# Kernel optimization log

Measured on AMD Instinct MI355X. Metric: run time of the kernel, lower is better.

Reference implementation:

```python
import jax, jax.numpy as jnp
import numpy as np

B, N, E = 2, 50000, 800000
IN_CH, SP_CH, OUT_CH, EDGE_CH = 64, 16, 32, 1


def _xavier(k, shape):
    scale = (2.0 / (shape[0] + shape[1])) ** 0.5
    return jax.random.normal(k, shape, dtype=jnp.float32) * scale


def setup_inputs() -> dict:
    key = jax.random.key(0)
    ks = jax.random.split(key, 20)
    return {
        "X": jax.random.normal(ks[0], (B, N, IN_CH), dtype=jnp.float32),
        "edge_index0": jax.random.randint(ks[1], (2, E), 0, N),
        "edge_index1": jax.random.randint(ks[2], (2, E), 0, N),
        "edge_weight0": jax.random.uniform(ks[3], (E, EDGE_CH), dtype=jnp.float32),
        "edge_weight1": jax.random.uniform(ks[4], (E, EDGE_CH), dtype=jnp.float32),
        "res_n_id0": jnp.arange(N),
        "res_n_id1": jnp.arange(N),
        # conv1 params (in=IN_CH, out=SP_CH)
        "value1": _xavier(ks[5], (IN_CH, SP_CH)),
        "key1": _xavier(ks[6], (SP_CH, SP_CH)),
        "query1": _xavier(ks[7], (SP_CH, SP_CH)),
        "we1": _xavier(ks[8], (EDGE_CH, SP_CH)),
        "att_w1": _xavier(ks[9], (3 * SP_CH, 1)),
        "att_b1": jnp.zeros((1,), jnp.float32),
        "cat_w1": _xavier(ks[10], (2 * SP_CH, SP_CH)),
        "cat_b1": jnp.zeros((SP_CH,), jnp.float32),
        # conv2 params (in=SP_CH, out=OUT_CH)
        "value2": _xavier(ks[11], (SP_CH, OUT_CH)),
        "key2": _xavier(ks[12], (OUT_CH, OUT_CH)),
        "query2": _xavier(ks[13], (OUT_CH, OUT_CH)),
        "we2": _xavier(ks[14], (EDGE_CH, OUT_CH)),
        "att_w2": _xavier(ks[15], (3 * OUT_CH, 1)),
        "att_b2": jnp.zeros((1,), jnp.float32),
        "cat_w2": _xavier(ks[16], (2 * OUT_CH, OUT_CH)),
        "cat_b2": jnp.zeros((OUT_CH,), jnp.float32),
    }


def _egnn_conv(Xs, Xd, ei, ef, value, key_w, query_w, we, att_w, att_b, cat_w, cat_b):
    # Xs: [B,Ns,Cin] source nodes, Xd: [B,Nd,Cin] dest nodes, ei: [2,E], ef: [E,edge_ch]
    xs = Xs @ value                       # [B,Ns,C]
    xd = Xd @ value                       # [B,Nd,C]
    e = ef @ we                           # [E,C]
    xj = xs[:, ei[0]]                     # [B,E,C] source gather
    xi = xd[:, ei[1]]                     # [B,E,C] dest gather
    q = xj @ query_w                      # note: original code names are swapped; kept faithful
    k = xi @ key_w
    att_in = jnp.concatenate([k, q, jnp.broadcast_to(e, q.shape)], axis=-1)  # [B,E,3C]
    att = jax.nn.sigmoid(att_in @ att_w + att_b)      # [B,E,1]
    msg = att * xj * jax.nn.sigmoid(e)                # [B,E,C]
    aggr = jnp.zeros(xd.shape, xd.dtype).at[:, ei[1]].add(msg)  # scatter-add over dest
    upd = jnp.concatenate([xd, aggr], axis=-1) @ cat_w + cat_b  # [B,Nd,C]
    return xd + jax.nn.relu(upd)


def reference(X, edge_index0, edge_index1, edge_weight0, edge_weight1,
              res_n_id0, res_n_id1,
              value1, key1, query1, we1, att_w1, att_b1, cat_w1, cat_b1,
              value2, key2, query2, we2, att_w2, att_b2, cat_w2, cat_b2):
    X1 = _egnn_conv(X, X[:, res_n_id0], edge_index0, edge_weight0,
                    value1, key1, query1, we1, att_w1, att_b1, cat_w1, cat_b1)
    X1 = jax.nn.leaky_relu(X1)  # negative_slope 0.01, matches torch default
    X2 = _egnn_conv(X1, X1[:, res_n_id1], edge_index1, edge_weight1,
                    value2, key2, query2, we2, att_w2, att_b2, cat_w2, cat_b2)
    return X2
```

## Files before the change

kernel.cpp:

```cpp
#include <hip/hip_runtime.h>
#include <hip/hip_fp16.h>

#define BB   2
#define NN   50000
#define EE   800000
#define INCH 64
#define C1   16
#define C2   32
#define NB   (BB*NN)

#define W1S   6
#define W2S   5
#define NBK1  ((NN + 63) >> 6)
#define NBK2  ((NN + 31) >> 5)
#define NBKT  (NBK1 + NBK2)
#define EB    4096
#define TPB   1024
#define NEBLK ((2*EE + EB - 1) / EB)

#define OFF_XS1   0
#define OFF_XS2   (OFF_XS1 + NB*C1/2)
#define OFF_DOTK1 (OFF_XS2 + NB*C2/2)
#define OFF_DOTQ1 (OFF_DOTK1 + NB)
#define OFF_DOTK2 (OFF_DOTQ1 + NB)
#define OFF_DOTQ2 (OFF_DOTK2 + NB)
#define OFF_AG1   (OFF_DOTQ2 + NB)
#define OFF_AG2   (OFF_AG1 + NN*32)
#define OFF_BTOT  (OFF_AG2 + NN*64)
#define OFF_BBASE (OFF_BTOT + NBKT)
#define OFF_START (OFF_BBASE + NBKT)
#define OFF_DEG   (OFF_START + 2*NN)
#define OFF_SC    (OFF_DEG + 2*NN)
#define OFF_RECS2 (OFF_SC + 2)
#define OFF_REGION (OFF_RECS2 + 2*EE*2)
#define OFF_RECS   OFF_REGION
#define OFF_BCNT   (OFF_REGION + 2*EE*2)
#define OFF_PREC   OFF_REGION

__device__ __forceinline__ float sigmoidf(float x) {
    return __builtin_amdgcn_rcpf(1.0f + __expf(-x));
}

__device__ __forceinline__ float h2f_u(unsigned u) {
    return __half2float(__ushort_as_half((unsigned short)u));
}

__global__ __launch_bounds__(TPB) void k_value1cnt(
        const float* __restrict__ X, const float* __restrict__ value1,
        const float* __restrict__ key1, const float* __restrict__ query1,
        const float* __restrict__ aw1,
        const int* __restrict__ ei0, const int* __restrict__ ei1,
        const float* __restrict__ we1, const float* __restrict__ we2,
        const float* __restrict__ aw2,
        __half* __restrict__ xs1h, float* __restrict__ dotk1,
        float* __restrict__ dotq1, unsigned* __restrict__ blockCnt,
        float* __restrict__ sc) {
    __shared__ float W[INCH*C1];
    __shared__ float KV[C1], QV[C1];
    __shared__ unsigned h[NBKT];
    int tid = threadIdx.x;
    if (tid < 256) {
        for (int i = tid; i < INCH*C1; i += 256) W[i] = value1[i];
        if (tid < C1) {
            float kv = 0.f, qv = 0.f;
#pragma unroll
            for (int j = 0; j < C1; ++j) {
                kv += key1[tid*C1+j]   * aw1[j];
                qv += query1[tid*C1+j] * aw1[C1+j];
            }
            KV[tid] = kv; QV[tid] = qv;
        }
    } else {
        for (int i = tid - 256; i < NBKT; i += 768) h[i] = 0u;
        if (blockIdx.x == 0 && tid == 256) {
            float e = 0.f;
            for (int j = 0; j < C1; ++j) e += we1[j] * aw1[2*C1+j];
            sc[0] = e;
        }
        if (blockIdx.x == 0 && tid == 257) {
            float e = 0.f;
            for (int j = 0; j < C2; ++j) e += we2[j] * aw2[2*C2+j];
            sc[1] = e;
        }
    }
    __syncthreads();
    if (tid < 256) {
        int bn = blockIdx.x * 256 + tid;
        if (bn < NB) {
            int b = (bn >= NN) ? 1 : 0;
            int node = bn - b*NN;
            const float4* Xr = (const float4*)(X + (size_t)bn * INCH);
            float acc[C1];
#pragma unroll
            for (int j = 0; j < C1; ++j) acc[j] = 0.f;
#pragma unroll
            for (int v = 0; v < 16; ++v) {
                float4 p = Xr[v];
                float x4[4] = {p.x, p.y, p.z, p.w};
#pragma unroll
                for (int hh = 0; hh < 4; ++hh) {
                    int i = v*4 + hh;
                    float xv = x4[hh];
#pragma unroll
                    for (int j = 0; j < C1; ++j) acc[j] += xv * W[i*C1+j];
                }
            }
            float dk = 0.f, dq = 0.f;
#pragma unroll
            for (int j = 0; j < C1; ++j) { dk += acc[j]*KV[j]; dq += acc[j]*QV[j]; }
            __half* o = xs1h + ((size_t)node * C1) * 2 + b;
#pragma unroll
            for (int j = 0; j < C1; ++j) o[2*j] = __float2half_rn(acc[j]);
            dotk1[node*2 + b] = dk; dotq1[node*2 + b] = dq;
        }
    } else {
        int base = blockIdx.x * EB;
        for (int j = tid - 256; j < EB; j += 768) {
            int t = base + j;
            if (t < 2*EE) {
                int bkt;
                if (t < EE) { int dst = ei0[EE + t];      bkt = dst >> W1S; }
                else        { int dst = ei1[EE + t - EE]; bkt = NBK1 + (dst >> W2S); }
                atomicAdd(&h[bkt], 1u);
            }
        }
    }
    __syncthreads();
    unsigned* o = blockCnt + (size_t)blockIdx.x * NBKT;
    for (int i = tid; i < NBKT; i += TPB) o[i] = h[i];
}

__global__ __launch_bounds__(512) void k_scanBkt(
        unsigned* __restrict__ blockCnt, unsigned* __restrict__ bktTot) {
    __shared__ unsigned s[512];
    int tid = threadIdx.x;
    int bkt = blockIdx.x;
    unsigned v = (tid < NEBLK) ? blockCnt[(size_t)tid * NBKT + bkt] : 0u;
    s[tid] = v;
    __syncthreads();
    for (int o = 1; o < 512; o <<= 1) {
        unsigned t = (tid >= o) ? s[tid - o] : 0u;
        __syncthreads();
        s[tid] += t;
        __syncthreads();
    }
    if (tid < NEBLK) blockCnt[(size_t)tid * NBKT + bkt] = s[tid] - v;
    if (tid == 511) bktTot[bkt] = s[511];
}

__global__ __launch_bounds__(1024) void k_scanTot(
        const unsigned* __restrict__ bktTot, unsigned* __restrict__ bucketBase) {
    __shared__ unsigned s[1024];
    int tid = threadIdx.x;
    int base = tid * 3;
    unsigned a0 = (base + 0 < NBKT) ? bktTot[base + 0] : 0u;
    unsigned a1 = (base + 1 < NBKT) ? bktTot[base + 1] : 0u;
    unsigned a2 = (base + 2 < NBKT) ? bktTot[base + 2] : 0u;
    unsigned l = a0 + a1 + a2;
    s[tid] = l;
    __syncthreads();
    for (int o = 1; o < 1024; o <<= 1) {
        unsigned t = (tid >= o) ? s[tid - o] : 0u;
        __syncthreads();
        s[tid] += t;
        __syncthreads();
    }
    unsigned ex = s[tid] - l;
    if (base + 0 < NBKT) bucketBase[base + 0] = ex;
    if (base + 1 < NBKT) bucketBase[base + 1] = ex + a0;
    if (base + 2 < NBKT) bucketBase[base + 2] = ex + a0 + a1;
}

__global__ __launch_bounds__(TPB) void k_permute(
        const int* __restrict__ ei0, const int* __restrict__ ei1,
        const float* __restrict__ ew0, const float* __restrict__ ew1,
        const unsigned* __restrict__ blockOff, const unsigned* __restrict__ bucketBase,
        uint2* __restrict__ recs) {
    __shared__ unsigned off[NBKT];
    __shared__ unsigned cur[NBKT];
    int tid = threadIdx.x;
    const unsigned* bo = blockOff + (size_t)blockIdx.x * NBKT;
    for (int i = tid; i < NBKT; i += TPB) { off[i] = bo[i] + bucketBase[i]; cur[i] = 0u; }
    __syncthreads();
    int base = blockIdx.x * EB;
#pragma unroll
    for (int j = 0; j < EB/TPB; ++j) {
        int t = base + j*TPB + tid;
        if (t >= 2*EE) break;
        int bkt, dl, src; float ef;
        if (t < EE) {
            int dst = ei0[EE + t];
            bkt = dst >> W1S; dl = dst & 63;
            src = ei0[t]; ef = ew0[t];
        } else {
            int e = t - EE;
            int dst = ei1[EE + e];
            bkt = NBK1 + (dst >> W2S); dl = dst & 31;
            src = ei1[e]; ef = ew1[e];
        }
        unsigned pos = off[bkt] + atomicAdd(&cur[bkt], 1u);
        recs[pos] = make_uint2((unsigned)src | ((unsigned)dl << 16), __float_as_uint(ef));
    }
}

__global__ __launch_bounds__(256) void k_sortbp(
        const uint2* __restrict__ recs, const unsigned* __restrict__ bktTot,
        const unsigned* __restrict__ bucketBase,
        const float* __restrict__ dotk1, const float* __restrict__ dotq1,
        const float* __restrict__ ab1, const float* __restrict__ sc,
        uint2* __restrict__ recs2, unsigned* __restrict__ startA,
        unsigned* __restrict__ degA) {
    __shared__ unsigned h[64], sOff[64], cur[64];
    int tid = threadIdx.x;
    int bkt = blockIdx.x;
    int lay1 = (bkt < NBK1) ? 1 : 0;
    int ndl  = lay1 ? 64 : 32;
    int nodeBase = lay1 ? (bkt << W1S) : ((bkt - NBK1) << W2S);
    int layOff   = lay1 ? 0 : NN;
    if (tid < 64) h[tid] = 0u;
    __syncthreads();
    unsigned cnt = bktTot[bkt], base = bucketBase[bkt];
    for (unsigned i = tid; i < cnt; i += 256)
        atomicAdd(&h[recs[base + i].x >> 16], 1u);
    __syncthreads();
    if (tid == 0) {
        unsigned run = 0;
        for (int d = 0; d < ndl; ++d) { sOff[d] = run; run += h[d]; }
    }
    __syncthreads();
    if (tid < ndl) {
        cur[tid] = sOff[tid];
        int node = nodeBase + tid;
        if (node < NN) {
            startA[layOff + node] = base + sOff[tid];
            degA[layOff + node]   = h[tid];
        }
    }
    __syncthreads();
    float ec = sc[0], ab0 = ab1[0];
    for (unsigned i = tid; i < cnt; i += 256) {
        uint2 r = recs[base + i];
        unsigned dl  = r.x >> 16;
        unsigned src = r.x & 0xffffu;
        unsigned pos = atomicAdd(&cur[dl], 1u);
        unsigned dst = (unsigned)nodeBase + dl;
        if (lay1) {
            float ef = __uint_as_float(r.y);
            float eb = ef * ec + ab0;
            float2 dk = *(const float2*)(dotk1 + dst*2);
            float2 dq = *(const float2*)(dotq1 + src*2);
            float p0 = sigmoidf(dk.x + dq.x + eb);
            float p1 = sigmoidf(dk.y + dq.y + eb);
            unsigned pu = __builtin_bit_cast(unsigned, __floats2half2_rn(p0, p1));
            unsigned eu = (unsigned)__half_as_ushort(__float2half_rn(ef));
            recs2[base + pos] = make_uint2(src | (pu << 16),
                                           (pu >> 16) | (eu << 16));
        } else {
            recs2[base + pos] = make_uint2(src | (dst << 16), r.y);
        }
    }
}

__global__ __launch_bounds__(256) void k_prep(
        const uint2* __restrict__ recs2seg, const float* __restrict__ dotk,
        const float* __restrict__ dotq, const float* __restrict__ ab,
        const float* __restrict__ sc, int scIdx, uint2* __restrict__ prec) {
    int e = blockIdx.x * 256 + threadIdx.x;
    uint2 r = recs2seg[e];
    int src = r.x & 0xffff, dst = r.x >> 16;
    float ef = __uint_as_float(r.y);
    float eb = ef * sc[scIdx] + ab[0];
    float2 dk = *(const float2*)(dotk + dst*2);
    float2 dq = *(const float2*)(dotq + src*2);
    float p0 = sigmoidf(dk.x + dq.x + eb);
    float p1 = sigmoidf(dk.y + dq.y + eb);
    unsigned pu = __builtin_bit_cast(unsigned, __floats2half2_rn(p0, p1));
    unsigned eu = (unsigned)__half_as_ushort(__float2half_rn(ef));
    prec[e] = make_uint2((unsigned)src | (pu << 16),
                         (pu >> 16) | (eu << 16));
}

__global__ __launch_bounds__(256) void k_aggr1u(
        const uint2* __restrict__ prec, const float* __restrict__ we,
        const uint2* __restrict__ xsh,
        const unsigned* __restrict__ startA, const unsigned* __restrict__ degA,
        const float* __restrict__ cat_w, const float* __restrict__ cat_b,
        const float* __restrict__ value2,
        const float* __restrict__ key2, const float* __restrict__ query2,
        const float* __restrict__ aw2, const __half* __restrict__ xs1h,
        __half* __restrict__ xs2h, float* __restrict__ dotk2,
        float* __restrict__ dotq2) {
    __shared__ float CW[2*C1*C1];
    __shared__ float CB[C1];
    __shared__ float V2[C1*C2];
    __shared__ float KV[C2], QV[C2];
    __shared__ float agS[16*36];
    __shared__ float xdS[16*2*17];
    __shared__ float x1S[16*2*17];
    int tid = threadIdx.x;
    for (int i = tid; i < 2*C1*C1; i += 256) CW[i] = cat_w[i];
    for (int i = tid; i < C1*C2;   i += 256) V2[i] = value2[i];
    if (tid < C1) CB[tid] = cat_b[tid];
    if (tid < C2) {
        float kv = 0.f;
#pragma unroll
        for (int j = 0; j < C2; ++j) kv += key2[tid*C2+j] * aw2[j];
        KV[tid] = kv;
    } else if (tid < 2*C2) {
        int c = tid - C2;
        float qv = 0.f;
#pragma unroll
        for (int j = 0; j < C2; ++j) qv += query2[c*C2+j] * aw2[C2+j];
        QV[c] = qv;
    }

    int nl = tid >> 4, sub = tid & 15, cp = sub & 7, h = sub >> 3;
    int node = blockIdx.x * 16 + nl;
    unsigned s = startA[node];
    unsigned n = degA[node];
    float w0 = we[2*cp], w1 = we[2*cp+1];
    float a0 = 0.f, a1 = 0.f, a2 = 0.f, a3 = 0.f;
    unsigned i = (unsigned)h;
    uint2 r_n = make_uint2(0u, 0u); uint2 xr_n = make_uint2(0u, 0u);
    if (i < n) {
        r_n  = prec[s + i];
        xr_n = xsh[(size_t)(r_n.x & 0xffff)*8 + cp];
    }
    for (; i < n; i += 2) {
        uint2 r = r_n; uint2 xr = xr_n;
        if (i + 2 < n) {
            r_n  = prec[s + i + 2];
            xr_n = xsh[(size_t)(r_n.x & 0xffff)*8 + cp];
        }
        float p0 = h2f_u(r.x >> 16);
        float p1 = h2f_u(r.y & 0xffff);
        float ef = h2f_u(r.y >> 16);
        float se0 = sigmoidf(ef * w0);
        float se1 = sigmoidf(ef * w1);
        float2 f0 = __half22float2(__builtin_bit_cast(__half2, xr.x));
        float2 f1 = __half22float2(__builtin_bit_cast(__half2, xr.y));
        a0 += p0 * se0 * f0.x;
        a1 += p1 * se0 * f0.y;
        a2 += p0 * se1 * f1.x;
        a3 += p1 * se1 * f1.y;
    }
    a0 += __shfl_xor(a0, 8); a1 += __shfl_xor(a1, 8);
    a2 += __shfl_xor(a2, 8); a3 += __shfl_xor(a3, 8);
    if (h == 0)
        ((float4*)(agS + nl*36))[cp] = make_float4(a0, a1, a2, a3);

    {
        unsigned w = ((const unsigned*)(xs1h))[(size_t)(blockIdx.x*16) * 16 + tid];
        int snl = tid >> 4, sc_ = tid & 15;
        xdS[(snl*2 + 0)*17 + sc_] = h2f_u(w);
        xdS[(snl*2 + 1)*17 + sc_] = h2f_u(w >> 16);
    }
    __syncthreads();

    int b  = (tid >> 3) & 1;
    int kk = tid & 7;
    const float* xdp = &xdS[(nl*2 + b)*17];
    const float* agp = &agS[nl*36];
    {
        int j0 = kk, j1 = kk + 8;
        float u0 = CB[j0], u1 = CB[j1];
#pragma unroll
        for (int i2 = 0; i2 < C1; ++i2) {
            float xv = xdp[i2];
            float av = agp[(i2>>1)*4 + (i2&1)*2 + b];
            u0 += xv * CW[i2*C1 + j0] + av * CW[(C1+i2)*C1 + j0];
            u1 += xv * CW[i2*C1 + j1] + av * CW[(C1+i2)*C1 + j1];
        }
        float o0 = xdp[j0] + fmaxf(u0, 0.f);
        float o1 = xdp[j1] + fmaxf(u1, 0.f);
        float* x1p = &x1S[(nl*2 + b)*17];
        x1p[j0] = (o0 > 0.f) ? o0 : 0.01f * o0;
        x1p[j1] = (o1 > 0.f) ? o1 : 0.01f * o1;
    }
    __syncthreads();
    {
        const float* x1p = &x1S[(nl*2 + b)*17];
        float dk = 0.f, dq = 0.f;
        __half* orow = xs2h + (size_t)node * C2 * 2 + b;
#pragma unroll
        for (int kq = 0; kq < 4; ++kq) {
            int k = kk + kq*8;
            float o2 = 0.f;
#pragma unroll
            for (int j = 0; j < C1; ++j) o2 += x1p[j] * V2[j*C2 + k];
            orow[2*k] = __float2half_rn(o2);
            dk += o2 * KV[k]; dq += o2 * QV[k];
        }
        dk += __shfl_xor(dk, 1); dq += __shfl_xor(dq, 1);
        dk += __shfl_xor(dk, 2); dq += __shfl_xor(dq, 2);
        dk += __shfl_xor(dk, 4); dq += __shfl_xor(dq, 4);
        if (kk == 0) { dotk2[node*2 + b] = dk; dotq2[node*2 + b] = dq; }
    }
}

__global__ __launch_bounds__(256) void k_aggr2u(
        const uint2* __restrict__ prec, const float* __restrict__ we,
        const uint2* __restrict__ xsh,
        const unsigned* __restrict__ startA, const unsigned* __restrict__ degA,
        const float* __restrict__ cat_w, const float* __restrict__ cat_b,
        const __half* __restrict__ xs2h, float* __restrict__ out) {
    __shared__ float CW[2*C2*C2];
    __shared__ float CB[C2];
    __shared__ float agS[8*68];
    __shared__ float xdS[8*2*33];
    int tid = threadIdx.x;
    for (int i = tid; i < 2*C2*C2; i += 256) CW[i] = cat_w[i];
    if (tid < C2) CB[tid] = cat_b[tid];

    int nl = tid >> 5, sub = tid & 31, cp = sub & 15, h = sub >> 4;
    int node = blockIdx.x * 8 + nl;
    unsigned s = startA[NN + node] - EE;
    unsigned n = degA[NN + node];
    float w0 = we[2*cp], w1 = we[2*cp+1];
    float a0 = 0.f, a1 = 0.f, a2 = 0.f, a3 = 0.f;
    unsigned i = (unsigned)h;
    uint2 r_n = make_uint2(0u, 0u); uint2 xr_n = make_uint2(0u, 0u);
    if (i < n) {
        r_n  = prec[s + i];
        xr_n = xsh[(size_t)(r_n.x & 0xffff)*16 + cp];
    }
    for (; i < n; i += 2) {
        uint2 r = r_n; uint2 xr = xr_n;
        if (i + 2 < n) {
            r_n  = prec[s + i + 2];
            xr_n = xsh[(size_t)(r_n.x & 0xffff)*16 + cp];
        }
        float p0 = h2f_u(r.x >> 16);
        float p1 = h2f_u(r.y & 0xffff);
        float ef = h2f_u(r.y >> 16);
        float se0 = sigmoidf(ef * w0);
        float se1 = sigmoidf(ef * w1);
        float2 f0 = __half22float2(__builtin_bit_cast(__half2, xr.x));
        float2 f1 = __half22float2(__builtin_bit_cast(__half2, xr.y));
        a0 += p0 * se0 * f0.x;
        a1 += p1 * se0 * f0.y;
        a2 += p0 * se1 * f1.x;
        a3 += p1 * se1 * f1.y;
    }
    a0 += __shfl_xor(a0, 16); a1 += __shfl_xor(a1, 16);
    a2 += __shfl_xor(a2, 16); a3 += __shfl_xor(a3, 16);
    if (h == 0)
        ((float4*)(agS + nl*68))[cp] = make_float4(a0, a1, a2, a3);

    {
        unsigned w = ((const unsigned*)(xs2h))[(size_t)(blockIdx.x*8) * 32 + tid];
        int snl = tid >> 5, sc_ = tid & 31;
        xdS[(snl*2 + 0)*33 + sc_] = h2f_u(w);
        xdS[(snl*2 + 1)*33 + sc_] = h2f_u(w >> 16);
    }
    __syncthreads();

    int b  = (tid >> 4) & 1;
    int kk = tid & 15;
    const float* xdp = &xdS[(nl*2 + b)*33];
    const float* agp = &agS[nl*68];
    float u0 = CB[kk], u1 = CB[kk+16];
#pragma unroll
    for (int ii = 0; ii < C2; ++ii) {
        float xv = xdp[ii];
        float av = agp[(ii>>1)*4 + (ii&1)*2 + b];
        u0 += xv * CW[ii*C2 + kk]        + av * CW[(C2+ii)*C2 + kk];
        u1 += xv * CW[ii*C2 + kk + 16]   + av * CW[(C2+ii)*C2 + kk + 16];
    }
    float o0 = xdp[kk]    + fmaxf(u0, 0.f);
    float o1 = xdp[kk+16] + fmaxf(u1, 0.f);
    float* orow = out + ((size_t)(b*NN + node)) * C2;
    orow[kk]      = o0;
    orow[kk + 16] = o1;
}

extern "C" void kernel_launch(void* const* d_in, const int* in_sizes, int n_in,
                              void* d_out, int out_size, void* d_ws, size_t ws_size,
                              hipStream_t stream) {
    const float* X      = (const float*)d_in[0];
    const int*   ei0    = (const int*)d_in[1];
    const int*   ei1    = (const int*)d_in[2];
    const float* ew0    = (const float*)d_in[3];
    const float* ew1    = (const float*)d_in[4];
    const float* value1 = (const float*)d_in[7];
    const float* key1   = (const float*)d_in[8];
    const float* query1 = (const float*)d_in[9];
    const float* we1    = (const float*)d_in[10];
    const float* aw1    = (const float*)d_in[11];
    const float* ab1    = (const float*)d_in[12];
    const float* cw1    = (const float*)d_in[13];
    const float* cb1    = (const float*)d_in[14];
    const float* value2 = (const float*)d_in[15];
    const float* key2   = (const float*)d_in[16];
    const float* query2 = (const float*)d_in[17];
    const float* we2    = (const float*)d_in[18];
    const float* aw2    = (const float*)d_in[19];
    const float* ab2    = (const float*)d_in[20];
    const float* cw2    = (const float*)d_in[21];
    const float* cb2    = (const float*)d_in[22];
    float* ws  = (float*)d_ws;
    float* out = (float*)d_out;

    __half* xs1h = (__half*)(ws + OFF_XS1);
    __half* xs2h = (__half*)(ws + OFF_XS2);
    unsigned* blockCnt   = (unsigned*)(ws + OFF_BCNT);
    unsigned* bktTot     = (unsigned*)(ws + OFF_BTOT);
    unsigned* bucketBase = (unsigned*)(ws + OFF_BBASE);
    unsigned* startA     = (unsigned*)(ws + OFF_START);
    unsigned* degA       = (unsigned*)(ws + OFF_DEG);
    uint2*    recs2      = (uint2*)(ws + OFF_RECS2);
    uint2*    recs       = (uint2*)(ws + OFF_RECS);
    uint2*    prec2      = (uint2*)(ws + OFF_PREC);

    k_value1cnt<<<NEBLK, TPB, 0, stream>>>(X, value1, key1, query1, aw1,
                                           ei0, ei1, we1, we2, aw2,
                                           xs1h, ws + OFF_DOTK1, ws + OFF_DOTQ1,
                                           blockCnt, ws + OFF_SC);

    k_scanBkt<<<NBKT, 512, 0, stream>>>(blockCnt, bktTot);
    k_scanTot<<<1, 1024, 0, stream>>>(bktTot, bucketBase);
    k_permute<<<NEBLK, TPB, 0, stream>>>(ei0, ei1, ew0, ew1,
                                         blockCnt, bucketBase, recs);
    k_sortbp<<<NBKT, 256, 0, stream>>>(recs, bktTot, bucketBase,
                                       ws + OFF_DOTK1, ws + OFF_DOTQ1,
                                       ab1, ws + OFF_SC,
                                       recs2, startA, degA);

    k_aggr1u<<<NN/16, 256, 0, stream>>>(recs2, we1, (const uint2*)xs1h,
                                        startA, degA, cw1, cb1,
                                        value2, key2, query2, aw2, xs1h,
                                        xs2h, ws + OFF_DOTK2, ws + OFF_DOTQ2);

    k_prep<<<EE/256, 256, 0, stream>>>(recs2 + EE, ws + OFF_DOTK2, ws + OFF_DOTQ2,
                                       ab2, ws + OFF_SC, 1, prec2);
    k_aggr2u<<<NN/8, 256, 0, stream>>>(prec2, we2, (const uint2*)xs2h,
                                       startA, degA, cw2, cb2, xs2h, out);
}
```

Before: 289.5 us.

## Defer layer-2 bucket sort into a fused sort+attention-prep kernel, deepen gather prefetch

The layer-2 half of the bucket sort moves out of k_sortbp into a new kernel, k_sortp2, which runs after layer-1 aggregation. It computes the layer-2 attention probabilities while sorting and writes packed records straight into recs2, so the separate k_prep pass and its intermediate write/read of 800K records are gone. The aggregation loops also prefetch the edge record two iterations ahead instead of one, to hide gather latency. The cost is an extra kernel launch in place of k_prep, and the recs region must stay intact until layer 2, which it does because k_prep no longer reuses it.

After: 285.8 us. No clear change (-1.3%).

```diff
diff --git a/kernel.cpp b/kernel.cpp
--- a/kernel.cpp
+++ b/kernel.cpp
@@ -35,7 +35,6 @@
 #define OFF_REGION (OFF_RECS2 + 2*EE*2)
 #define OFF_RECS   OFF_REGION
 #define OFF_BCNT   (OFF_REGION + 2*EE*2)
-#define OFF_PREC   OFF_REGION
 
 __device__ __forceinline__ float sigmoidf(float x) {
     return __builtin_amdgcn_rcpf(1.0f + __expf(-x));
@@ -213,10 +212,7 @@
     __shared__ unsigned h[64], sOff[64], cur[64];
     int tid = threadIdx.x;
     int bkt = blockIdx.x;
-    int lay1 = (bkt < NBK1) ? 1 : 0;
-    int ndl  = lay1 ? 64 : 32;
-    int nodeBase = lay1 ? (bkt << W1S) : ((bkt - NBK1) << W2S);
-    int layOff   = lay1 ? 0 : NN;
+    int nodeBase = bkt << W1S;
     if (tid < 64) h[tid] = 0u;
     __syncthreads();
     unsigned cnt = bktTot[bkt], base = bucketBase[bkt];
@@ -225,15 +221,15 @@
     __syncthreads();
     if (tid == 0) {
         unsigned run = 0;
-        for (int d = 0; d < ndl; ++d) { sOff[d] = run; run += h[d]; }
-    }
-    __syncthreads();
-    if (tid < ndl) {
+        for (int d = 0; d < 64; ++d) { sOff[d] = run; run += h[d]; }
+    }
+    __syncthreads();
+    if (tid < 64) {
         cur[tid] = sOff[tid];
         int node = nodeBase + tid;
         if (node < NN) {
-            startA[layOff + node] = base + sOff[tid];
-            degA[layOff + node]   = h[tid];
+            startA[node] = base + sOff[tid];
+            degA[node]   = h[tid];
         }
     }
     __syncthreads();
@@ -244,40 +240,68 @@
         unsigned src = r.x & 0xffffu;
         unsigned pos = atomicAdd(&cur[dl], 1u);
         unsigned dst = (unsigned)nodeBase + dl;
-        if (lay1) {
-            float ef = __uint_as_float(r.y);
-            float eb = ef * ec + ab0;
-            float2 dk = *(const float2*)(dotk1 + dst*2);
-            float2 dq = *(const float2*)(dotq1 + src*2);
-            float p0 = sigmoidf(dk.x + dq.x + eb);
-            float p1 = sigmoidf(dk.y + dq.y + eb);
-            unsigned pu = __builtin_bit_cast(unsigned, __floats2half2_rn(p0, p1));
-            unsigned eu = (unsigned)__half_as_ushort(__float2half_rn(ef));
-            recs2[base + pos] = make_uint2(src | (pu << 16),
-                                           (pu >> 16) | (eu << 16));
-        } else {
-            recs2[base + pos] = make_uint2(src | (dst << 16), r.y);
-        }
-    }
-}
-
-__global__ __launch_bounds__(256) void k_prep(
-        const uint2* __restrict__ recs2seg, const float* __restrict__ dotk,
-        const float* __restrict__ dotq, const float* __restrict__ ab,
-        const float* __restrict__ sc, int scIdx, uint2* __restrict__ prec) {
-    int e = blockIdx.x * 256 + threadIdx.x;
-    uint2 r = recs2seg[e];
-    int src = r.x & 0xffff, dst = r.x >> 16;
-    float ef = __uint_as_float(r.y);
-    float eb = ef * sc[scIdx] + ab[0];
-    float2 dk = *(const float2*)(dotk + dst*2);
-    float2 dq = *(const float2*)(dotq + src*2);
-    float p0 = sigmoidf(dk.x + dq.x + eb);
-    float p1 = sigmoidf(dk.y + dq.y + eb);
-    unsigned pu = __builtin_bit_cast(unsigned, __floats2half2_rn(p0, p1));
-    unsigned eu = (unsigned)__half_as_ushort(__float2half_rn(ef));
-    prec[e] = make_uint2((unsigned)src | (pu << 16),
-                         (pu >> 16) | (eu << 16));
+        float ef = __uint_as_float(r.y);
+        float eb = ef * ec + ab0;
+        float2 dk = *(const float2*)(dotk1 + dst*2);
+        float2 dq = *(const float2*)(dotq1 + src*2);
+        float p0 = sigmoidf(dk.x + dq.x + eb);
+        float p1 = sigmoidf(dk.y + dq.y + eb);
+        unsigned pu = __builtin_bit_cast(unsigned, __floats2half2_rn(p0, p1));
+        unsigned eu = (unsigned)__half_as_ushort(__float2half_rn(ef));
+        recs2[base + pos] = make_uint2(src | (pu << 16),
+                                       (pu >> 16) | (eu << 16));
+    }
+}
+
+__global__ __launch_bounds__(256) void k_sortp2(
+        const uint2* __restrict__ recs, const unsigned* __restrict__ bktTot,
+        const unsigned* __restrict__ bucketBase,
+        const float* __restrict__ dotk2, const float* __restrict__ dotq2,
+        const float* __restrict__ ab2, const float* __restrict__ sc,
+        uint2* __restrict__ recs2, unsigned* __restrict__ startA,
+        unsigned* __restrict__ degA) {
+    __shared__ unsigned h[32], sOff[32], cur[32];
+    int tid = threadIdx.x;
+    int bkt = NBK1 + blockIdx.x;
+    int nodeBase = blockIdx.x << W2S;
+    if (tid < 32) h[tid] = 0u;
+    __syncthreads();
+    unsigned cnt = bktTot[bkt], base = bucketBase[bkt];
+    for (unsigned i = tid; i < cnt; i += 256)
+        atomicAdd(&h[recs[base + i].x >> 16], 1u);
+    __syncthreads();
+    if (tid == 0) {
+        unsigned run = 0;
+        for (int d = 0; d < 32; ++d) { sOff[d] = run; run += h[d]; }
+    }
+    __syncthreads();
+    if (tid < 32) {
+        cur[tid] = sOff[tid];
+        int node = nodeBase + tid;
+        if (node < NN) {
+            startA[NN + node] = base + sOff[tid];
+            degA[NN + node]   = h[tid];
+        }
+    }
+    __syncthreads();
+    float ec = sc[1], ab0 = ab2[0];
+    for (unsigned i = tid; i < cnt; i += 256) {
+        uint2 r = recs[base + i];
+        unsigned dl  = r.x >> 16;
+        unsigned src = r.x & 0xffffu;
+        unsigned pos = atomicAdd(&cur[dl], 1u);
+        unsigned dst = (unsigned)nodeBase + dl;
+        float ef = __uint_as_float(r.y);
+        float eb = ef * ec + ab0;
+        float2 dk = *(const float2*)(dotk2 + dst*2);
+        float2 dq = *(const float2*)(dotq2 + src*2);
+        float p0 = sigmoidf(dk.x + dq.x + eb);
+        float p1 = sigmoidf(dk.y + dq.y + eb);
+        unsigned pu = __builtin_bit_cast(unsigned, __floats2half2_rn(p0, p1));
+        unsigned eu = (unsigned)__half_as_ushort(__float2half_rn(ef));
+        recs2[base + pos] = make_uint2(src | (pu << 16),
+                                       (pu >> 16) | (eu << 16));
+    }
 }
 
 __global__ __launch_bounds__(256) void k_aggr1u(
@@ -321,17 +345,15 @@
     float w0 = we[2*cp], w1 = we[2*cp+1];
     float a0 = 0.f, a1 = 0.f, a2 = 0.f, a3 = 0.f;
     unsigned i = (unsigned)h;
-    uint2 r_n = make_uint2(0u, 0u); uint2 xr_n = make_uint2(0u, 0u);
-    if (i < n) {
-        r_n  = prec[s + i];
-        xr_n = xsh[(size_t)(r_n.x & 0xffff)*8 + cp];
-    }
+    uint2 rA = make_uint2(0u,0u), rB = make_uint2(0u,0u), xrA = make_uint2(0u,0u);
+    if (i < n)     rA  = prec[s + i];
+    if (i + 2 < n) rB  = prec[s + i + 2];
+    if (i < n)     xrA = xsh[(size_t)(rA.x & 0xffff)*8 + cp];
     for (; i < n; i += 2) {
-        uint2 r = r_n; uint2 xr = xr_n;
-        if (i + 2 < n) {
-            r_n  = prec[s + i + 2];
-            xr_n = xsh[(size_t)(r_n.x & 0xffff)*8 + cp];
-        }
+        uint2 r = rA, xr = xrA;
+        rA = rB;
+        if (i + 4 < n) rB = prec[s + i + 4];
+        if (i + 2 < n) xrA = xsh[(size_t)(rA.x & 0xffff)*8 + cp];
         float p0 = h2f_u(r.x >> 16);
         float p1 = h2f_u(r.y & 0xffff);
         float ef = h2f_u(r.y >> 16);
@@ -414,22 +436,20 @@
 
     int nl = tid >> 5, sub = tid & 31, cp = sub & 15, h = sub >> 4;
     int node = blockIdx.x * 8 + nl;
-    unsigned s = startA[NN + node] - EE;
+    unsigned s = startA[NN + node];
     unsigned n = degA[NN + node];
     float w0 = we[2*cp], w1 = we[2*cp+1];
     float a0 = 0.f, a1 = 0.f, a2 = 0.f, a3 = 0.f;
     unsigned i = (unsigned)h;
-    uint2 r_n = make_uint2(0u, 0u); uint2 xr_n = make_uint2(0u, 0u);
-    if (i < n) {
-        r_n  = prec[s + i];
-        xr_n = xsh[(size_t)(r_n.x & 0xffff)*16 + cp];
-    }
+    uint2 rA = make_uint2(0u,0u), rB = make_uint2(0u,0u), xrA = make_uint2(0u,0u);
+    if (i < n)     rA  = prec[s + i];
+    if (i + 2 < n) rB  = prec[s + i + 2];
+    if (i < n)     xrA = xsh[(size_t)(rA.x & 0xffff)*16 + cp];
     for (; i < n; i += 2) {
-        uint2 r = r_n; uint2 xr = xr_n;
-        if (i + 2 < n) {
-            r_n  = prec[s + i + 2];
-            xr_n = xsh[(size_t)(r_n.x & 0xffff)*16 + cp];
-        }
+        uint2 r = rA, xr = xrA;
+        rA = rB;
+        if (i + 4 < n) rB = prec[s + i + 4];
+        if (i + 2 < n) xrA = xsh[(size_t)(rA.x & 0xffff)*16 + cp];
         float p0 = h2f_u(r.x >> 16);
         float p1 = h2f_u(r.y & 0xffff);
         float ef = h2f_u(r.y >> 16);
@@ -510,7 +530,6 @@
     unsigned* degA       = (unsigned*)(ws + OFF_DEG);
     uint2*    recs2      = (uint2*)(ws + OFF_RECS2);
     uint2*    recs       = (uint2*)(ws + OFF_RECS);
-    uint2*    prec2      = (uint2*)(ws + OFF_PREC);
 
     k_value1cnt<<<NEBLK, TPB, 0, stream>>>(X, value1, key1, query1, aw1,
                                            ei0, ei1, we1, we2, aw2,
@@ -521,7 +540,7 @@
     k_scanTot<<<1, 1024, 0, stream>>>(bktTot, bucketBase);
     k_permute<<<NEBLK, TPB, 0, stream>>>(ei0, ei1, ew0, ew1,
                                          blockCnt, bucketBase, recs);
-    k_sortbp<<<NBKT, 256, 0, stream>>>(recs, bktTot, bucketBase,
+    k_sortbp<<<NBK1, 256, 0, stream>>>(recs, bktTot, bucketBase,
                                        ws + OFF_DOTK1, ws + OFF_DOTQ1,
                                        ab1, ws + OFF_SC,
                                        recs2, startA, degA);
@@ -531,8 +550,11 @@
                                         value2, key2, query2, aw2, xs1h,
                                         xs2h, ws + OFF_DOTK2, ws + OFF_DOTQ2);
 
-    k_prep<<<EE/256, 256, 0, stream>>>(recs2 + EE, ws + OFF_DOTK2, ws + OFF_DOTQ2,
-                                       ab2, ws + OFF_SC, 1, prec2);
-    k_aggr2u<<<NN/8, 256, 0, stream>>>(prec2, we2, (const uint2*)xs2h,
+    k_sortp2<<<NBK2, 256, 0, stream>>>(recs, bktTot, bucketBase,
+                                       ws + OFF_DOTK2, ws + OFF_DOTQ2,
+                                       ab2, ws + OFF_SC,
+                                       recs2, startA, degA);
+
+    k_aggr2u<<<NN/8, 256, 0, stream>>>(recs2, we2, (const uint2*)xs2h,
                                        startA, degA, cw2, cb2, xs2h, out);
 }
```
